# Kernel optimization log

Hardware: AMD Instinct MI355X
Metric: run time of the kernel (lower is better)

## Reference

```python
import jax, jax.numpy as jnp
import numpy as np

B, L, DM, H, DK, DV = 4, 1024, 1024, 16, 64, 64


def setup_inputs() -> dict:
    key = jax.random.key(0)
    ks = jax.random.split(key, 9)
    s = 0.02
    q = jax.random.normal(ks[0], (B, L, DM), jnp.float32)
    k = jax.random.normal(ks[1], (B, L, DM), jnp.float32)
    v = jax.random.normal(ks[2], (B, L, DM), jnp.float32)
    # causal mask: True = masked out
    attn_mask = jnp.broadcast_to(jnp.triu(jnp.ones((L, L), bool), k=1), (B, L, L))
    w_q = jax.random.normal(ks[3], (DM, H * DK), jnp.float32) * s
    w_k = jax.random.normal(ks[4], (DM, H * DK), jnp.float32) * s
    w_v = jax.random.normal(ks[5], (DM, H * DV), jnp.float32) * s
    w_o = jax.random.normal(ks[6], (H * DV, DM), jnp.float32) * s
    ln_g = jnp.ones((DM,), jnp.float32)
    ln_b = jnp.zeros((DM,), jnp.float32)
    return {"q": q, "k": k, "v": v, "w_q": w_q, "w_k": w_k, "w_v": w_v,
            "w_o": w_o, "ln_g": ln_g, "ln_b": ln_b,
            "attn_mask": attn_mask, "n_head": H}


def _mha(q, k, v, w_q, w_k, w_v, w_o, ln_g, ln_b, attn_mask, n_head):
    b, lq, dm = q.shape
    lk = k.shape[1]
    d_k = w_q.shape[1] // n_head
    d_v = w_v.shape[1] // n_head
    temper = jnp.asarray(np.sqrt(dm), q.dtype)  # NOTE: sqrt(d_model), as in source
    residual = q
    # faithful to source: flat .view reshape (b, l, h*d) -> (b*h, l, d), NO transpose
    qh = (q @ w_q).reshape(b * n_head, lq, d_k)
    kh = (k @ w_k).reshape(b * n_head, lk, d_k)
    vh = (v @ w_v).reshape(b * n_head, lk, d_v)
    attn = jnp.einsum('bqd,bkd->bqk', qh, kh) / temper  # (b*h, lq, lk)
    mask_r = jnp.tile(attn_mask, (n_head, 1, 1))
    attn = jnp.where(mask_r, -jnp.inf, attn)
    attn = jax.nn.softmax(attn, axis=-1)
    out = jnp.einsum('bqk,bkd->bqd', attn, vh)  # (b*h, lq, d_v)
    out = out.reshape(b, lq, n_head * d_v)
    out = out @ w_o + residual  # dropout = identity (eval)
    mu = jnp.mean(out, axis=-1, keepdims=True)
    var = jnp.mean(jnp.square(out - mu), axis=-1, keepdims=True)
    out = (out - mu) * jax.lax.rsqrt(var + 1e-6) * ln_g + ln_b
    return out, attn


def reference(q, k, v, w_q, w_k, w_v, w_o, ln_g, ln_b, attn_mask, n_head):
    return _mha(q, k, v, w_q, w_k, w_v, w_o, ln_g, ln_b, attn_mask, n_head)
```

## Files before the change

### kernel.cpp

```cpp
#include <hip/hip_runtime.h>
#include <stdint.h>

typedef unsigned short u16;
typedef __attribute__((ext_vector_type(8))) short bf16x8;
typedef __attribute__((ext_vector_type(4))) float f32x4;
typedef __attribute__((ext_vector_type(4))) unsigned short us4;

#define MFMA_BF16(a, b, c) __builtin_amdgcn_mfma_f32_16x16x32_bf16((a), (b), (c), 0, 0, 0)

__device__ __forceinline__ u16 f2bf(float f) {
  uint32_t u = __builtin_bit_cast(uint32_t, f);
  u += 0x7fffu + ((u >> 16) & 1u);
  return (u16)(u >> 16);
}

__device__ __forceinline__ void async_copy16(void* lds, const void* g) {
  __builtin_amdgcn_global_load_lds(
      (const __attribute__((address_space(1))) unsigned int*)g,
      (__attribute__((address_space(3))) unsigned int*)lds, 16, 0, 0);
}

__global__ __launch_bounds__(256) void k_pre(const float* __restrict__ q,
                                             const float* __restrict__ k,
                                             const float* __restrict__ v,
                                             const float* __restrict__ w0,
                                             const float* __restrict__ w1,
                                             const float* __restrict__ w2,
                                             const float* __restrict__ w3,
                                             us4* __restrict__ qkvb,
                                             u16* __restrict__ wT) {
  __shared__ float t[32][33];
  int bid = blockIdx.x;
  int tid = threadIdx.x;
  if (bid < 12288) {
    int z = bid >> 12;
    const float4* src = (z == 0) ? (const float4*)q : (z == 1) ? (const float4*)k : (const float4*)v;
    int i = (bid & 4095) * 256 + tid;
    float4 val = src[i];
    us4 o;
    o[0] = f2bf(val.x); o[1] = f2bf(val.y); o[2] = f2bf(val.z); o[3] = f2bf(val.w);
    qkvb[(size_t)z * 1048576 + i] = o;
  } else {
    int w = bid - 12288;
    int z = w >> 10, r_ = w & 1023;
    int bx = r_ & 31, by = r_ >> 5;
    const float* W = (z == 0) ? w0 : (z == 1) ? w1 : (z == 2) ? w2 : w3;
    u16* WT = wT + (size_t)z * 1048576;
    int c = tid & 31, r0 = tid >> 5;
#pragma unroll
    for (int i = 0; i < 4; ++i) {
      int r = r0 + i * 8;
      t[r][c] = W[(size_t)(by * 32 + r) * 1024 + bx * 32 + c];
    }
    __syncthreads();
#pragma unroll
    for (int i = 0; i < 4; ++i) {
      int r = r0 + i * 8;
      WT[(size_t)(bx * 32 + r) * 1024 + by * 32 + c] = f2bf(t[c][r]);
    }
  }
}

__global__ __launch_bounds__(256) void k_vtrans(const u16* __restrict__ VP, u16* __restrict__ VT) {
  int jt = blockIdx.x;
  int bh = blockIdx.y;
  __shared__ u16 t[64][65];
  int tid = threadIdx.x;
  const u16* src = VP + (size_t)bh * 65536 + (size_t)jt * 64 * 64;
#pragma unroll
  for (int i = 0; i < 16; ++i) {
    int e = tid + i * 256;
    t[e >> 6][e & 63] = src[e];
  }
  __syncthreads();
  u16* dst = VT + (size_t)bh * 65536 + jt * 64;
#pragma unroll
  for (int i = 0; i < 16; ++i) {
    int e = tid + i * 256;
    int d = e >> 6, j = e & 63;
    dst[(size_t)d * 1024 + j] = t[j][d];
  }
}

__global__ __launch_bounds__(256) void k_gemm_bt(const u16* __restrict__ A,
                                                 const u16* __restrict__ BT,
                                                 u16* __restrict__ Cb, float* __restrict__ Cf,
                                                 const float* __restrict__ res,
                                                 int N, int K, int mode, int wgrp) {
  __shared__ __align__(16) u16 SM[4][4096];
  int bm, bn;
  {
    int wg = blockIdx.x + blockIdx.y * gridDim.x;
    int per = gridDim.y >> 3;
    int xcd = wg & 7;
    int idx = wg >> 3;
    bm = xcd * per + (idx % per);
    bn = idx / per;
  }
  int tid = threadIdx.x;
  int wave = tid >> 6, lane = tid & 63;
  int wr = wave >> 1, wc = wave & 1;
  int fl = lane & 15, fg = lane >> 4;
  f32x4 acc[4][4] = {};

  const char* Abase = (const char*)(A + (size_t)bm * 128 * K);
  const char* Bbase = (const char*)(BT + (wgrp ? (size_t)(bm >> 5) * 1048576 : 0) +
                                    (size_t)bn * 128 * K);
  int off = wave * 1024 + lane * 16;

#define GSTAGE(buf, kt)                                                              \
  {                                                                                  \
    _Pragma("unroll") for (int is = 0; is < 2; ++is) {                               \
      int o = is * 4096 + off;                                                       \
      int row = o >> 6, cb = o & 63;                                                 \
      async_copy16((char*)SM[buf] + is * 4096 + wave * 1024,                         \
                   Abase + (size_t)row * (K * 2) + (kt) * 2 + cb);                   \
      async_copy16((char*)SM[2 + (buf)] + is * 4096 + wave * 1024,                   \
                   Bbase + (size_t)row * (K * 2) + (kt) * 2 + cb);                   \
    }                                                                                \
  }

  GSTAGE(0, 0);
  __syncthreads();
  int cur = 0;
  for (int kt = 0; kt < K; kt += 32) {
    if (kt + 32 < K) GSTAGE(cur ^ 1, kt + 32);
    bf16x8 af[4], bfr[4];
#pragma unroll
    for (int m = 0; m < 4; ++m)
      af[m] = *(const bf16x8*)((const char*)SM[cur] + (wr * 64 + m * 16 + fl) * 64 + fg * 16);
#pragma unroll
    for (int n = 0; n < 4; ++n)
      bfr[n] = *(const bf16x8*)((const char*)SM[2 + cur] + (wc * 64 + n * 16 + fl) * 64 + fg * 16);
#pragma unroll
    for (int m = 0; m < 4; ++m)
#pragma unroll
      for (int n = 0; n < 4; ++n)
        acc[m][n] = MFMA_BF16(af[m], bfr[n], acc[m][n]);
    __syncthreads();
    cur ^= 1;
  }
#undef GSTAGE

  float* EP = (float*)&SM[0][0] + wave * 2048;
  int colbase = bn * 128 + wc * 64;
#pragma unroll
  for (int m = 0; m < 4; ++m) {
    int rowbase = bm * 128 + wr * 64 + m * 16;
#pragma unroll
    for (int n = 0; n < 4; ++n)
#pragma unroll
      for (int r = 0; r < 4; ++r)
        EP[(fg * 4 + r) * 68 + n * 16 + fl] = acc[m][n][r];
    if (mode) {
#pragma unroll
      for (int j = 0; j < 4; ++j) {
        int row = (lane >> 4) + 4 * j;
        int colf = (lane & 15) * 4;
        float4 val = *(const float4*)(&EP[row * 68 + colf]);
        size_t gidx = (size_t)(rowbase + row) * N + colbase + colf;
        float4 rr = *(const float4*)(res + gidx);
        val.x += rr.x; val.y += rr.y; val.z += rr.z; val.w += rr.w;
        *(float4*)(Cf + gidx) = val;
      }
    } else {
#pragma unroll
      for (int j = 0; j < 2; ++j) {
        int row = (lane >> 3) + 8 * j;
        int colf = (lane & 7) * 8;
        const float* s = &EP[row * 68 + colf];
        us4 lo, hi;
#pragma unroll
        for (int i = 0; i < 4; ++i) { lo[i] = f2bf(s[i]); hi[i] = f2bf(s[4 + i]); }
        u16* d = Cb + (size_t)(rowbase + row) * N + colbase + colf;
        *(us4*)d = lo;
        *(us4*)(d + 4) = hi;
      }
    }
  }
}

__global__ __launch_bounds__(256) void k_gemm_out64(const u16* __restrict__ A,
                                                    const u16* __restrict__ BT,
                                                    float* __restrict__ Cf,
                                                    const float* __restrict__ res) {
  __shared__ __align__(16) u16 SM[12288];
  char* base = (char*)SM;
  int bm, bn;
  {
    int wg = blockIdx.x + blockIdx.y * 8;
    int xcd = wg & 7, idx = wg >> 3;
    bm = xcd * 8 + (idx & 7);
    bn = idx >> 3;
  }
  int tid = threadIdx.x;
  int wave = tid >> 6, lane = tid & 63;
  int wr = wave >> 1, wc = wave & 1;
  int fl = lane & 15, fg = lane >> 4;
  f32x4 acc[2][4] = {};

  const char* Abase = (const char*)(A + (size_t)bm * 65536);
  const char* Bbase = (const char*)(BT + (size_t)bn * 131072);

#define OSTAGE(buf, kt)                                                          \
  {                                                                              \
    int oA = wave * 1024 + lane * 16;                                            \
    int rowA = oA >> 6, cbA = oA & 63;                                           \
    async_copy16(base + (buf) * 4096 + wave * 1024,                              \
                 Abase + (size_t)rowA * 2048 + (kt) * 2 + cbA);                  \
    _Pragma("unroll") for (int is = 0; is < 2; ++is) {                           \
      int oB = is * 4096 + wave * 1024 + lane * 16;                              \
      int rowB = oB >> 6, cbB = oB & 63;                                         \
      async_copy16(base + 8192 + (buf) * 8192 + is * 4096 + wave * 1024,         \
                   Bbase + (size_t)rowB * 2048 + (kt) * 2 + cbB);                \
    }                                                                            \
  }

  OSTAGE(0, 0);
  __syncthreads();
  int cur = 0;
  for (int kt = 0; kt < 1024; kt += 32) {
    if (kt + 32 < 1024) OSTAGE(cur ^ 1, kt + 32);
    const char* Ab = base + cur * 4096;
    const char* Bb = base + 8192 + cur * 8192;
    bf16x8 af[2], bfr[4];
#pragma unroll
    for (int m = 0; m < 2; ++m)
      af[m] = *(const bf16x8*)(Ab + (wr * 32 + m * 16 + fl) * 64 + fg * 16);
#pragma unroll
    for (int n = 0; n < 4; ++n)
      bfr[n] = *(const bf16x8*)(Bb + (wc * 64 + n * 16 + fl) * 64 + fg * 16);
#pragma unroll
    for (int m = 0; m < 2; ++m)
#pragma unroll
      for (int n = 0; n < 4; ++n)
        acc[m][n] = MFMA_BF16(af[m], bfr[n], acc[m][n]);
    __syncthreads();
    cur ^= 1;
  }
#undef OSTAGE

  float* EP = (float*)base + wave * 1088;
  int colbase = bn * 128 + wc * 64;
#pragma unroll
  for (int m = 0; m < 2; ++m) {
    int rowbase = bm * 64 + wr * 32 + m * 16;
#pragma unroll
    for (int n = 0; n < 4; ++n)
#pragma unroll
      for (int r = 0; r < 4; ++r)
        EP[(fg * 4 + r) * 68 + n * 16 + fl] = acc[m][n][r];
#pragma unroll
    for (int j = 0; j < 4; ++j) {
      int row = (lane >> 4) + 4 * j;
      int colf = (lane & 15) * 4;
      float4 val = *(const float4*)(&EP[row * 68 + colf]);
      size_t gidx = (size_t)(rowbase + row) * 1024 + colbase + colf;
      float4 rr = *(const float4*)(res + gidx);
      val.x += rr.x; val.y += rr.y; val.z += rr.z; val.w += rr.w;
      *(float4*)(Cf + gidx) = val;
    }
  }
}

__global__ __launch_bounds__(256) void k_attn(const u16* __restrict__ QP,
                                              const u16* __restrict__ KP,
                                              const u16* __restrict__ VT,
                                              float* __restrict__ attn,
                                              u16* __restrict__ AO) {
  int bh = blockIdx.x;
  int qb = 15 - blockIdx.y;
  int tid = threadIdx.x;
  int wave = tid >> 6, lane = tid & 63;
  int fl = lane & 15, fg = lane >> 4;
  int qw = qb * 64 + wave * 16;

  const u16* Qb = QP + (size_t)bh * 65536;
  const char* Kbyte = (const char*)(KP + (size_t)bh * 65536);
  const u16* Vb = VT + (size_t)bh * 65536;
  float* Ab = attn + (size_t)bh * 1048576;

  __shared__ __align__(16) u16 Ks[2][4096];
  __shared__ __align__(16) float Ps[4][16][36];
  __shared__ __align__(16) u16 Pt[4][16][64];

#define KSTAGE(buf, jt)                                                                 \
  {                                                                                     \
    _Pragma("unroll") for (int c2 = 0; c2 < 2; ++c2) {                                  \
      int o = c2 * 4096 + wave * 1024 + lane * 16;                                      \
      int row = o >> 7, col = o & 127;                                                  \
      async_copy16((char*)Ks[buf] + c2 * 4096 + wave * 1024,                            \
                   Kbyte + (size_t)((jt) * 64 + row) * 128 + (col ^ ((row & 7) << 4))); \
    }                                                                                   \
  }

  bf16x8 qf0 = *(const bf16x8*)(Qb + (size_t)(qw + fl) * 64 + fg * 8);
  bf16x8 qf1 = *(const bf16x8*)(Qb + (size_t)(qw + fl) * 64 + 32 + fg * 8);

  float den[4] = {0.f, 0.f, 0.f, 0.f};

  KSTAGE(0, 0);
  __syncthreads();
  int cur = 0;
  for (int jt = 0; jt <= qb; ++jt) {
    if (jt < qb) KSTAGE(cur ^ 1, jt + 1);
    int j0 = jt * 64;
    f32x4 c[4] = {};
#pragma unroll
    for (int n = 0; n < 4; ++n) {
      int r = n * 16 + fl;
      bf16x8 k0 = *(const bf16x8*)((const char*)Ks[cur] + r * 128 + ((fg * 16) ^ ((r & 7) << 4)));
      bf16x8 k1 = *(const bf16x8*)((const char*)Ks[cur] + r * 128 + ((64 + fg * 16) ^ ((r & 7) << 4)));
      c[n] = MFMA_BF16(qf0, k0, c[n]);
      c[n] = MFMA_BF16(qf1, k1, c[n]);
    }
#pragma unroll
    for (int r = 0; r < 4; ++r) {
      int row = qw + fg * 4 + r;
      float sum = 0.f;
#pragma unroll
      for (int n = 0; n < 4; ++n) {
        int col = j0 + n * 16 + fl;
        sum += (col > row) ? 0.f : __expf(c[n][r] * 0.03125f);
      }
#pragma unroll
      for (int o2 = 1; o2 < 16; o2 <<= 1) sum += __shfl_xor(sum, o2);
      den[r] += sum;
    }
    __syncthreads();
    cur ^= 1;
  }

  float invden[4];
#pragma unroll
  for (int r = 0; r < 4; ++r) invden[r] = 1.0f / den[r];

  f32x4 oacc[4] = {};

  KSTAGE(0, 0);
  __syncthreads();
  cur = 0;
  for (int jt = 0; jt <= qb; ++jt) {
    if (jt < qb) KSTAGE(cur ^ 1, jt + 1);
    int j0 = jt * 64;
    f32x4 c[4] = {};
#pragma unroll
    for (int n = 0; n < 4; ++n) {
      int r = n * 16 + fl;
      bf16x8 k0 = *(const bf16x8*)((const char*)Ks[cur] + r * 128 + ((fg * 16) ^ ((r & 7) << 4)));
      bf16x8 k1 = *(const bf16x8*)((const char*)Ks[cur] + r * 128 + ((64 + fg * 16) ^ ((r & 7) << 4)));
      c[n] = MFMA_BF16(qf0, k0, c[n]);
      c[n] = MFMA_BF16(qf1, k1, c[n]);
    }
    bf16x8 vf0[4], vf1[4];
#pragma unroll
    for (int n = 0; n < 4; ++n) {
      const u16* vp = Vb + (size_t)(n * 16 + fl) * 1024 + j0;
      vf0[n] = *(const bf16x8*)(vp + fg * 8);
      vf1[n] = *(const bf16x8*)(vp + 32 + fg * 8);
    }
    float pv_[4][4];
#pragma unroll
    for (int r = 0; r < 4; ++r) {
      int row = qw + fg * 4 + r;
#pragma unroll
      for (int n = 0; n < 4; ++n) {
        int col = j0 + n * 16 + fl;
        pv_[n][r] = (col > row) ? 0.f : __expf(c[n][r] * 0.03125f) * invden[r];
      }
    }
#pragma unroll
    for (int t = 0; t < 2; ++t) {
#pragma unroll
      for (int n2 = 0; n2 < 2; ++n2)
#pragma unroll
        for (int r = 0; r < 4; ++r)
          Ps[wave][fg * 4 + r][n2 * 16 + fl] = pv_[t * 2 + n2][r];
#pragma unroll
      for (int i = 0; i < 2; ++i) {
        int idx = i * 64 + lane;
        int r16 = idx >> 3, f4 = idx & 7;
        float4 val = *(const float4*)(&Ps[wave][r16][f4 * 4]);
        *(float4*)(Ab + (size_t)(qw + r16) * 1024 + j0 + t * 32 + f4 * 4) = val;
      }
    }
#pragma unroll
    for (int r = 0; r < 4; ++r)
#pragma unroll
      for (int n = 0; n < 4; ++n)
        Pt[wave][fg * 4 + r][n * 16 + fl] = f2bf(pv_[n][r]);
    bf16x8 pa0 = *(const bf16x8*)(&Pt[wave][fl][fg * 8]);
    bf16x8 pa1 = *(const bf16x8*)(&Pt[wave][fl][32 + fg * 8]);
#pragma unroll
    for (int n = 0; n < 4; ++n) {
      oacc[n] = MFMA_BF16(pa0, vf0[n], oacc[n]);
      oacc[n] = MFMA_BF16(pa1, vf1[n], oacc[n]);
    }
    __syncthreads();
    cur ^= 1;
  }
#undef KSTAGE

  float4 z; z.x = 0.f; z.y = 0.f; z.z = 0.f; z.w = 0.f;
  for (int jt = qb + 1; jt < 16; ++jt) {
    int j0 = jt * 64;
#pragma unroll
    for (int i = 0; i < 4; ++i) {
      int idx = i * 64 + lane;
      int r16 = idx >> 4, f4 = idx & 15;
      *(float4*)(Ab + (size_t)(qw + r16) * 1024 + j0 + f4 * 4) = z;
    }
  }

#pragma unroll
  for (int n = 0; n < 4; ++n)
#pragma unroll
    for (int r = 0; r < 4; ++r)
      Pt[wave][fg * 4 + r][n * 16 + fl] = f2bf(oacc[n][r]);
#pragma unroll
  for (int j = 0; j < 2; ++j) {
    int row = (lane >> 3) + 8 * j;
    int colf = (lane & 7) * 8;
    bf16x8 val = *(const bf16x8*)(&Pt[wave][row][colf]);
    *(bf16x8*)(AO + (size_t)bh * 65536 + (size_t)(qw + row) * 64 + colf) = val;
  }
}

__global__ __launch_bounds__(256) void k_lnorm(float* __restrict__ io,
                                               const float* __restrict__ g,
                                               const float* __restrict__ b) {
  int row = blockIdx.x, tid = threadIdx.x;
  float* p = io + (size_t)row * 1024 + tid * 4;
  float4 x = *(const float4*)p;
  float s1 = x.x + x.y + x.z + x.w;
  float s2 = x.x * x.x + x.y * x.y + x.z * x.z + x.w * x.w;
#pragma unroll
  for (int o = 1; o < 64; o <<= 1) {
    s1 += __shfl_xor(s1, o);
    s2 += __shfl_xor(s2, o);
  }
  __shared__ float r1[4], r2[4];
  int wave = tid >> 6;
  if ((tid & 63) == 0) { r1[wave] = s1; r2[wave] = s2; }
  __syncthreads();
  s1 = r1[0] + r1[1] + r1[2] + r1[3];
  s2 = r2[0] + r2[1] + r2[2] + r2[3];
  float mu = s1 * (1.0f / 1024.0f);
  float var = s2 * (1.0f / 1024.0f) - mu * mu;
  float rs = rsqrtf(var + 1e-6f);
  float4 gg = *(const float4*)(g + tid * 4);
  float4 bb = *(const float4*)(b + tid * 4);
  float4 y;
  y.x = (x.x - mu) * rs * gg.x + bb.x;
  y.y = (x.y - mu) * rs * gg.y + bb.y;
  y.z = (x.z - mu) * rs * gg.z + bb.z;
  y.w = (x.w - mu) * rs * gg.w + bb.w;
  *(float4*)p = y;
}

extern "C" void kernel_launch(void* const* d_in, const int* in_sizes, int n_in,
                              void* d_out, int out_size, void* d_ws, size_t ws_size,
                              hipStream_t stream) {
  const float* q = (const float*)d_in[0];
  const float* k = (const float*)d_in[1];
  const float* v = (const float*)d_in[2];
  const float* w_q = (const float*)d_in[3];
  const float* w_k = (const float*)d_in[4];
  const float* w_v = (const float*)d_in[5];
  const float* w_o = (const float*)d_in[6];
  const float* ln_g = (const float*)d_in[7];
  const float* ln_b = (const float*)d_in[8];

  float* out = (float*)d_out;
  float* attnp = out + 4194304;

  char* ws = (char*)d_ws;
  u16* QP = (u16*)(ws);
  u16* VP = (u16*)(ws + (16u << 20));
  u16* VT = (u16*)(ws + (24u << 20));
  u16* AO = (u16*)(ws + (32u << 20));
  u16* wT = (u16*)(ws + (40u << 20));
  u16* KP = QP + 4194304;
  u16* woT = wT + 3145728;

  u16* qkvb = (u16*)attnp;

  k_pre<<<16384, 256, 0, stream>>>(q, k, v, w_q, w_k, w_v, w_o, (us4*)qkvb, wT);

  k_gemm_bt<<<dim3(8, 96), 256, 0, stream>>>(qkvb, wT, QP, nullptr, nullptr, 1024, 1024, 0, 1);

  k_vtrans<<<dim3(16, 64), 256, 0, stream>>>(VP, VT);

  k_attn<<<dim3(64, 16), 256, 0, stream>>>(QP, KP, VT, attnp, AO);

  k_gemm_out64<<<dim3(8, 64), 256, 0, stream>>>(AO, woT, out, q);

  k_lnorm<<<4096, 256, 0, stream>>>(out, ln_g, ln_b);
}
```

Before: 160.3 us.

## Load K directly from global memory and drop LDS double-buffering in attention

Removes the LDS K staging (async global-to-LDS copies, double buffer, and per-tile __syncthreads) from both attention passes. Each wave now reads its K fragments straight from global memory, relying on L1/L2 reuse across the four waves. The V fragment loads move next to the PV MFMAs, and __expf(x/32) becomes exp2f(x*log2e/32). This removes barriers and LDS traffic but repeats global K reads per wave and exposes load latency with no explicit prefetch.

```diff
diff --git a/kernel.cpp b/kernel.cpp
--- a/kernel.cpp
+++ b/kernel.cpp
@@ -276,41 +276,28 @@
   int qw = qb * 64 + wave * 16;
 
   const u16* Qb = QP + (size_t)bh * 65536;
-  const char* Kbyte = (const char*)(KP + (size_t)bh * 65536);
+  const u16* Kb = KP + (size_t)bh * 65536;
   const u16* Vb = VT + (size_t)bh * 65536;
   float* Ab = attn + (size_t)bh * 1048576;
 
-  __shared__ __align__(16) u16 Ks[2][4096];
   __shared__ __align__(16) float Ps[4][16][36];
   __shared__ __align__(16) u16 Pt[4][16][64];
 
-#define KSTAGE(buf, jt)                                                                 \
-  {                                                                                     \
-    _Pragma("unroll") for (int c2 = 0; c2 < 2; ++c2) {                                  \
-      int o = c2 * 4096 + wave * 1024 + lane * 16;                                      \
-      int row = o >> 7, col = o & 127;                                                  \
-      async_copy16((char*)Ks[buf] + c2 * 4096 + wave * 1024,                            \
-                   Kbyte + (size_t)((jt) * 64 + row) * 128 + (col ^ ((row & 7) << 4))); \
-    }                                                                                   \
-  }
+  const float K2 = 0.045084220f;
 
   bf16x8 qf0 = *(const bf16x8*)(Qb + (size_t)(qw + fl) * 64 + fg * 8);
   bf16x8 qf1 = *(const bf16x8*)(Qb + (size_t)(qw + fl) * 64 + 32 + fg * 8);
 
   float den[4] = {0.f, 0.f, 0.f, 0.f};
 
-  KSTAGE(0, 0);
-  __syncthreads();
-  int cur = 0;
   for (int jt = 0; jt <= qb; ++jt) {
-    if (jt < qb) KSTAGE(cur ^ 1, jt + 1);
     int j0 = jt * 64;
     f32x4 c[4] = {};
 #pragma unroll
     for (int n = 0; n < 4; ++n) {
-      int r = n * 16 + fl;
-      bf16x8 k0 = *(const bf16x8*)((const char*)Ks[cur] + r * 128 + ((fg * 16) ^ ((r & 7) << 4)));
-      bf16x8 k1 = *(const bf16x8*)((const char*)Ks[cur] + r * 128 + ((64 + fg * 16) ^ ((r & 7) << 4)));
+      const u16* kp = Kb + (size_t)(j0 + n * 16 + fl) * 64;
+      bf16x8 k0 = *(const bf16x8*)(kp + fg * 8);
+      bf16x8 k1 = *(const bf16x8*)(kp + 32 + fg * 8);
       c[n] = MFMA_BF16(qf0, k0, c[n]);
       c[n] = MFMA_BF16(qf1, k1, c[n]);
     }
@@ -321,14 +308,12 @@
 #pragma unroll
       for (int n = 0; n < 4; ++n) {
         int col = j0 + n * 16 + fl;
-        sum += (col > row) ? 0.f : __expf(c[n][r] * 0.03125f);
+        sum += (col > row) ? 0.f : exp2f(c[n][r] * K2);
       }
 #pragma unroll
       for (int o2 = 1; o2 < 16; o2 <<= 1) sum += __shfl_xor(sum, o2);
       den[r] += sum;
     }
-    __syncthreads();
-    cur ^= 1;
   }
 
   float invden[4];
@@ -337,28 +322,17 @@
 
   f32x4 oacc[4] = {};
 
-  KSTAGE(0, 0);
-  __syncthreads();
-  cur = 0;
   for (int jt = 0; jt <= qb; ++jt) {
-    if (jt < qb) KSTAGE(cur ^ 1, jt + 1);
     int j0 = jt * 64;
     f32x4 c[4] = {};
 #pragma unroll
     for (int n = 0; n < 4; ++n) {
-      int r = n * 16 + fl;
-      bf16x8 k0 = *(const bf16x8*)((const char*)Ks[cur] + r * 128 + ((fg * 16) ^ ((r & 7) << 4)));
-      bf16x8 k1 = *(const bf16x8*)((const char*)Ks[cur] + r * 128 + ((64 + fg * 16) ^ ((r & 7) << 4)));
+      const u16* kp = Kb + (size_t)(j0 + n * 16 + fl) * 64;
+      bf16x8 k0 = *(const bf16x8*)(kp + fg * 8);
+      bf16x8 k1 = *(const bf16x8*)(kp + 32 + fg * 8);
       c[n] = MFMA_BF16(qf0, k0, c[n]);
       c[n] = MFMA_BF16(qf1, k1, c[n]);
     }
-    bf16x8 vf0[4], vf1[4];
-#pragma unroll
-    for (int n = 0; n < 4; ++n) {
-      const u16* vp = Vb + (size_t)(n * 16 + fl) * 1024 + j0;
-      vf0[n] = *(const bf16x8*)(vp + fg * 8);
-      vf1[n] = *(const bf16x8*)(vp + 32 + fg * 8);
-    }
     float pv_[4][4];
 #pragma unroll
     for (int r = 0; r < 4; ++r) {
@@ -366,7 +340,7 @@
 #pragma unroll
       for (int n = 0; n < 4; ++n) {
         int col = j0 + n * 16 + fl;
-        pv_[n][r] = (col > row) ? 0.f : __expf(c[n][r] * 0.03125f) * invden[r];
+        pv_[n][r] = (col > row) ? 0.f : exp2f(c[n][r] * K2) * invden[r];
       }
     }
 #pragma unroll
@@ -393,13 +367,13 @@
     bf16x8 pa1 = *(const bf16x8*)(&Pt[wave][fl][32 + fg * 8]);
 #pragma unroll
     for (int n = 0; n < 4; ++n) {
-      oacc[n] = MFMA_BF16(pa0, vf0[n], oacc[n]);
-      oacc[n] = MFMA_BF16(pa1, vf1[n], oacc[n]);
-    }
-    __syncthreads();
-    cur ^= 1;
-  }
-#undef KSTAGE
+      const u16* vp = Vb + (size_t)(n * 16 + fl) * 1024 + j0;
+      bf16x8 v0 = *(const bf16x8*)(vp + fg * 8);
+      bf16x8 v1 = *(const bf16x8*)(vp + 32 + fg * 8);
+      oacc[n] = MFMA_BF16(pa0, v0, oacc[n]);
+      oacc[n] = MFMA_BF16(pa1, v1, oacc[n]);
+    }
+  }
 
   float4 z; z.x = 0.f; z.y = 0.f; z.z = 0.f; z.w = 0.f;
   for (int jt = qb + 1; jt < 16; ++jt) {
```

Result: slower. 215.2 us (+34.2%).

## Overlap causal-mask zero-fill of attention output with the QKV projection GEMM

Applied to the files above, without the earlier changes.

The QKV GEMM grid gains extra blocks, interleaved among the GEMM tiles. These blocks zero the strictly-upper-triangular tiles of the attention-probability output for heads 6 and up, whose memory is not used as bf16 staging for the projection inputs. The attention kernel now zero-fills only heads 0–5, so most of the large store traffic overlaps with the compute-bound GEMM instead of running in the attention kernel. The GEMM is also specialised to fixed sizes, and the softmax uses exp2f with a folded log2(e)/32 constant instead of __expf. In exchange, the buffer aliasing becomes more fragile and the tile-to-XCD mapping gets more complex.

```diff
diff --git a/kernel.cpp b/kernel.cpp
--- a/kernel.cpp
+++ b/kernel.cpp
@@ -82,30 +82,47 @@
   }
 }
 
-__global__ __launch_bounds__(256) void k_gemm_bt(const u16* __restrict__ A,
-                                                 const u16* __restrict__ BT,
-                                                 u16* __restrict__ Cb, float* __restrict__ Cf,
-                                                 const float* __restrict__ res,
-                                                 int N, int K, int mode, int wgrp) {
+__global__ __launch_bounds__(256) void k_gemm_qkv(const u16* __restrict__ A,
+                                                  const u16* __restrict__ BT,
+                                                  u16* __restrict__ Cb,
+                                                  float* __restrict__ attnp) {
   __shared__ __align__(16) u16 SM[4][4096];
-  int bm, bn;
-  {
-    int wg = blockIdx.x + blockIdx.y * gridDim.x;
-    int per = gridDim.y >> 3;
-    int xcd = wg & 7;
-    int idx = wg >> 3;
-    bm = xcd * per + (idx % per);
-    bn = idx / per;
-  }
   int tid = threadIdx.x;
+  int wg = blockIdx.x + blockIdx.y * 8;
+  int xcd = wg & 7;
+  int idx = wg >> 3;
+  int gi_cur = (idx * 96) / 154;
+  int gi_next = ((idx + 1) * 96) / 154;
+  if (gi_next == gi_cur) {
+    int zi = idx - gi_cur;
+    int unit = xcd * 58 + zi;
+    int bh = 6 + (unit >> 3);
+    int s = unit & 7;
+    float* Ah = attnp + (size_t)bh * 1048576;
+    float4 z4; z4.x = 0.f; z4.y = 0.f; z4.z = 0.f; z4.w = 0.f;
+    for (int qb2 = 0; qb2 < 15; ++qb2)
+      for (int jt = qb2 + 1; jt < 16; ++jt) {
+        if (((qb2 * 16 + jt) & 7) != s) continue;
+        float* basez = Ah + (size_t)(qb2 * 64) * 1024 + jt * 64;
+#pragma unroll
+        for (int i = 0; i < 4; ++i) {
+          int id2 = i * 256 + tid;
+          int row = id2 >> 4, c16 = id2 & 15;
+          *(float4*)(basez + (size_t)row * 1024 + c16 * 4) = z4;
+        }
+      }
+    return;
+  }
+  int gi = gi_cur;
+  int bm = xcd * 12 + (gi % 12);
+  int bn = gi / 12;
   int wave = tid >> 6, lane = tid & 63;
   int wr = wave >> 1, wc = wave & 1;
   int fl = lane & 15, fg = lane >> 4;
   f32x4 acc[4][4] = {};
 
-  const char* Abase = (const char*)(A + (size_t)bm * 128 * K);
-  const char* Bbase = (const char*)(BT + (wgrp ? (size_t)(bm >> 5) * 1048576 : 0) +
-                                    (size_t)bn * 128 * K);
+  const char* Abase = (const char*)(A + (size_t)bm * 131072);
+  const char* Bbase = (const char*)(BT + (size_t)(bm >> 5) * 1048576 + (size_t)bn * 131072);
   int off = wave * 1024 + lane * 16;
 
 #define GSTAGE(buf, kt)                                                              \
@@ -114,17 +131,17 @@
       int o = is * 4096 + off;                                                       \
       int row = o >> 6, cb = o & 63;                                                 \
       async_copy16((char*)SM[buf] + is * 4096 + wave * 1024,                         \
-                   Abase + (size_t)row * (K * 2) + (kt) * 2 + cb);                   \
+                   Abase + (size_t)row * 2048 + (kt) * 2 + cb);                      \
       async_copy16((char*)SM[2 + (buf)] + is * 4096 + wave * 1024,                   \
-                   Bbase + (size_t)row * (K * 2) + (kt) * 2 + cb);                   \
+                   Bbase + (size_t)row * 2048 + (kt) * 2 + cb);                      \
     }                                                                                \
   }
 
   GSTAGE(0, 0);
   __syncthreads();
   int cur = 0;
-  for (int kt = 0; kt < K; kt += 32) {
-    if (kt + 32 < K) GSTAGE(cur ^ 1, kt + 32);
+  for (int kt = 0; kt < 1024; kt += 32) {
+    if (kt + 32 < 1024) GSTAGE(cur ^ 1, kt + 32);
     bf16x8 af[4], bfr[4];
 #pragma unroll
     for (int m = 0; m < 4; ++m)
@@ -152,30 +169,17 @@
 #pragma unroll
       for (int r = 0; r < 4; ++r)
         EP[(fg * 4 + r) * 68 + n * 16 + fl] = acc[m][n][r];
-    if (mode) {
-#pragma unroll
-      for (int j = 0; j < 4; ++j) {
-        int row = (lane >> 4) + 4 * j;
-        int colf = (lane & 15) * 4;
-        float4 val = *(const float4*)(&EP[row * 68 + colf]);
-        size_t gidx = (size_t)(rowbase + row) * N + colbase + colf;
-        float4 rr = *(const float4*)(res + gidx);
-        val.x += rr.x; val.y += rr.y; val.z += rr.z; val.w += rr.w;
-        *(float4*)(Cf + gidx) = val;
-      }
-    } else {
-#pragma unroll
-      for (int j = 0; j < 2; ++j) {
-        int row = (lane >> 3) + 8 * j;
-        int colf = (lane & 7) * 8;
-        const float* s = &EP[row * 68 + colf];
-        us4 lo, hi;
-#pragma unroll
-        for (int i = 0; i < 4; ++i) { lo[i] = f2bf(s[i]); hi[i] = f2bf(s[4 + i]); }
-        u16* d = Cb + (size_t)(rowbase + row) * N + colbase + colf;
-        *(us4*)d = lo;
-        *(us4*)(d + 4) = hi;
-      }
+#pragma unroll
+    for (int j = 0; j < 2; ++j) {
+      int row = (lane >> 3) + 8 * j;
+      int colf = (lane & 7) * 8;
+      const float* s = &EP[row * 68 + colf];
+      us4 lo, hi;
+#pragma unroll
+      for (int i = 0; i < 4; ++i) { lo[i] = f2bf(s[i]); hi[i] = f2bf(s[4 + i]); }
+      u16* d = Cb + (size_t)(rowbase + row) * 1024 + colbase + colf;
+      *(us4*)d = lo;
+      *(us4*)(d + 4) = hi;
     }
   }
 }
@@ -284,6 +288,8 @@
   __shared__ __align__(16) float Ps[4][16][36];
   __shared__ __align__(16) u16 Pt[4][16][64];
 
+  const float K2 = 0.045084220f;
+
 #define KSTAGE(buf, jt)                                                                 \
   {                                                                                     \
     _Pragma("unroll") for (int c2 = 0; c2 < 2; ++c2) {                                  \
@@ -321,7 +327,7 @@
 #pragma unroll
       for (int n = 0; n < 4; ++n) {
         int col = j0 + n * 16 + fl;
-        sum += (col > row) ? 0.f : __expf(c[n][r] * 0.03125f);
+        sum += (col > row) ? 0.f : exp2f(c[n][r] * K2);
       }
 #pragma unroll
       for (int o2 = 1; o2 < 16; o2 <<= 1) sum += __shfl_xor(sum, o2);
@@ -366,7 +372,7 @@
 #pragma unroll
       for (int n = 0; n < 4; ++n) {
         int col = j0 + n * 16 + fl;
-        pv_[n][r] = (col > row) ? 0.f : __expf(c[n][r] * 0.03125f) * invden[r];
+        pv_[n][r] = (col > row) ? 0.f : exp2f(c[n][r] * K2) * invden[r];
       }
     }
 #pragma unroll
@@ -401,14 +407,16 @@
   }
 #undef KSTAGE
 
-  float4 z; z.x = 0.f; z.y = 0.f; z.z = 0.f; z.w = 0.f;
-  for (int jt = qb + 1; jt < 16; ++jt) {
-    int j0 = jt * 64;
-#pragma unroll
-    for (int i = 0; i < 4; ++i) {
-      int idx = i * 64 + lane;
-      int r16 = idx >> 4, f4 = idx & 15;
-      *(float4*)(Ab + (size_t)(qw + r16) * 1024 + j0 + f4 * 4) = z;
+  if (bh < 6) {
+    float4 z; z.x = 0.f; z.y = 0.f; z.z = 0.f; z.w = 0.f;
+    for (int jt = qb + 1; jt < 16; ++jt) {
+      int j0 = jt * 64;
+#pragma unroll
+      for (int i = 0; i < 4; ++i) {
+        int idx = i * 64 + lane;
+        int r16 = idx >> 4, f4 = idx & 15;
+        *(float4*)(Ab + (size_t)(qw + r16) * 1024 + j0 + f4 * 4) = z;
+      }
     }
   }
 
@@ -487,7 +495,7 @@
 
   k_pre<<<16384, 256, 0, stream>>>(q, k, v, w_q, w_k, w_v, w_o, (us4*)qkvb, wT);
 
-  k_gemm_bt<<<dim3(8, 96), 256, 0, stream>>>(qkvb, wT, QP, nullptr, nullptr, 1024, 1024, 0, 1);
+  k_gemm_qkv<<<dim3(8, 154), 256, 0, stream>>>(qkvb, wT, QP, attnp);
 
   k_vtrans<<<dim3(16, 64), 256, 0, stream>>>(VP, VT);
 
```

After: 180.1 us. 12.4% more time.

## Fuse fp32-to-bf16 activation conversion into QKV GEMM and use exp2 softmax

Applied to the files above, without the earlier changes.

The separate pre-pass that converted q/k/v to bf16 is removed. The QKV GEMM now loads fp32 activation tiles directly into swizzled LDS and converts them to bf16 in registers with packed cvt instructions, so the intermediate bf16 activation buffer is never written or read back. The weight transpose becomes its own kernel. Separately, the softmax exponent uses exp2f with a folded log2e scale. In exchange, A-tile LDS traffic doubles and conversion ALU work moves into the GEMM inner loop.

```diff
diff --git a/kernel.cpp b/kernel.cpp
--- a/kernel.cpp
+++ b/kernel.cpp
@@ -20,44 +20,37 @@
       (__attribute__((address_space(3))) unsigned int*)lds, 16, 0, 0);
 }
 
-__global__ __launch_bounds__(256) void k_pre(const float* __restrict__ q,
-                                             const float* __restrict__ k,
-                                             const float* __restrict__ v,
-                                             const float* __restrict__ w0,
-                                             const float* __restrict__ w1,
-                                             const float* __restrict__ w2,
-                                             const float* __restrict__ w3,
-                                             us4* __restrict__ qkvb,
-                                             u16* __restrict__ wT) {
+__device__ __forceinline__ bf16x8 cvt8(f32x4 lo, f32x4 hi) {
+  union { bf16x8 v; uint32_t w[4]; } u;
+  asm("v_cvt_pk_bf16_f32 %0, %1, %2" : "=v"(u.w[0]) : "v"(lo[0]), "v"(lo[1]));
+  asm("v_cvt_pk_bf16_f32 %0, %1, %2" : "=v"(u.w[1]) : "v"(lo[2]), "v"(lo[3]));
+  asm("v_cvt_pk_bf16_f32 %0, %1, %2" : "=v"(u.w[2]) : "v"(hi[0]), "v"(hi[1]));
+  asm("v_cvt_pk_bf16_f32 %0, %1, %2" : "=v"(u.w[3]) : "v"(hi[2]), "v"(hi[3]));
+  return u.v;
+}
+
+__global__ __launch_bounds__(256) void k_pre_w(const float* __restrict__ w0,
+                                               const float* __restrict__ w1,
+                                               const float* __restrict__ w2,
+                                               const float* __restrict__ w3,
+                                               u16* __restrict__ wT) {
+  const float* W = (blockIdx.z == 0) ? w0 : (blockIdx.z == 1) ? w1
+                   : (blockIdx.z == 2) ? w2 : w3;
+  u16* WT = wT + (size_t)blockIdx.z * 1048576;
   __shared__ float t[32][33];
-  int bid = blockIdx.x;
+  int bx = blockIdx.x, by = blockIdx.y;
   int tid = threadIdx.x;
-  if (bid < 12288) {
-    int z = bid >> 12;
-    const float4* src = (z == 0) ? (const float4*)q : (z == 1) ? (const float4*)k : (const float4*)v;
-    int i = (bid & 4095) * 256 + tid;
-    float4 val = src[i];
-    us4 o;
-    o[0] = f2bf(val.x); o[1] = f2bf(val.y); o[2] = f2bf(val.z); o[3] = f2bf(val.w);
-    qkvb[(size_t)z * 1048576 + i] = o;
-  } else {
-    int w = bid - 12288;
-    int z = w >> 10, r_ = w & 1023;
-    int bx = r_ & 31, by = r_ >> 5;
-    const float* W = (z == 0) ? w0 : (z == 1) ? w1 : (z == 2) ? w2 : w3;
-    u16* WT = wT + (size_t)z * 1048576;
-    int c = tid & 31, r0 = tid >> 5;
-#pragma unroll
-    for (int i = 0; i < 4; ++i) {
-      int r = r0 + i * 8;
-      t[r][c] = W[(size_t)(by * 32 + r) * 1024 + bx * 32 + c];
-    }
-    __syncthreads();
-#pragma unroll
-    for (int i = 0; i < 4; ++i) {
-      int r = r0 + i * 8;
-      WT[(size_t)(bx * 32 + r) * 1024 + by * 32 + c] = f2bf(t[c][r]);
-    }
+  int c = tid & 31, r0 = tid >> 5;
+#pragma unroll
+  for (int i = 0; i < 4; ++i) {
+    int r = r0 + i * 8;
+    t[r][c] = W[(size_t)(by * 32 + r) * 1024 + bx * 32 + c];
+  }
+  __syncthreads();
+#pragma unroll
+  for (int i = 0; i < 4; ++i) {
+    int r = r0 + i * 8;
+    WT[(size_t)(bx * 32 + r) * 1024 + by * 32 + c] = f2bf(t[c][r]);
   }
 }
 
@@ -82,16 +75,17 @@
   }
 }
 
-__global__ __launch_bounds__(256) void k_gemm_bt(const u16* __restrict__ A,
-                                                 const u16* __restrict__ BT,
-                                                 u16* __restrict__ Cb, float* __restrict__ Cf,
-                                                 const float* __restrict__ res,
-                                                 int N, int K, int mode, int wgrp) {
-  __shared__ __align__(16) u16 SM[4][4096];
+__global__ __launch_bounds__(256) void k_gemm_qkv(const float* __restrict__ q,
+                                                  const float* __restrict__ k,
+                                                  const float* __restrict__ v,
+                                                  const u16* __restrict__ wT,
+                                                  u16* __restrict__ Cb) {
+  __shared__ __align__(16) float Asm[2][4096];
+  __shared__ __align__(16) u16 Bsm[2][4096];
   int bm, bn;
   {
-    int wg = blockIdx.x + blockIdx.y * gridDim.x;
-    int per = gridDim.y >> 3;
+    int wg = blockIdx.x + blockIdx.y * 8;
+    int per = 12;
     int xcd = wg & 7;
     int idx = wg >> 3;
     bm = xcd * per + (idx % per);
@@ -103,35 +97,51 @@
   int fl = lane & 15, fg = lane >> 4;
   f32x4 acc[4][4] = {};
 
-  const char* Abase = (const char*)(A + (size_t)bm * 128 * K);
-  const char* Bbase = (const char*)(BT + (wgrp ? (size_t)(bm >> 5) * 1048576 : 0) +
-                                    (size_t)bn * 128 * K);
-  int off = wave * 1024 + lane * 16;
-
-#define GSTAGE(buf, kt)                                                              \
-  {                                                                                  \
-    _Pragma("unroll") for (int is = 0; is < 2; ++is) {                               \
-      int o = is * 4096 + off;                                                       \
-      int row = o >> 6, cb = o & 63;                                                 \
-      async_copy16((char*)SM[buf] + is * 4096 + wave * 1024,                         \
-                   Abase + (size_t)row * (K * 2) + (kt) * 2 + cb);                   \
-      async_copy16((char*)SM[2 + (buf)] + is * 4096 + wave * 1024,                   \
-                   Bbase + (size_t)row * (K * 2) + (kt) * 2 + cb);                   \
-    }                                                                                \
-  }
-
-  GSTAGE(0, 0);
+  int z = bm >> 5;
+  const char* Abase = (const char*)((z == 0 ? q : z == 1 ? k : v) + (size_t)(bm & 31) * 131072);
+  const char* Bbase = (const char*)(wT + (size_t)z * 1048576 + (size_t)bn * 131072);
+
+#define ASTAGE(buf, kt)                                                             \
+  {                                                                                 \
+    _Pragma("unroll") for (int is = 0; is < 4; ++is) {                              \
+      int o = is * 4096 + wave * 1024 + lane * 16;                                  \
+      int row = o >> 7, cb = o & 127;                                               \
+      async_copy16((char*)Asm[buf] + is * 4096 + wave * 1024,                       \
+                   Abase + (size_t)row * 4096 + (kt) * 4 + (cb ^ ((row & 7) << 4))); \
+    }                                                                               \
+  }
+#define BSTAGE(buf, kt)                                                             \
+  {                                                                                 \
+    _Pragma("unroll") for (int is = 0; is < 2; ++is) {                              \
+      int o = is * 4096 + wave * 1024 + lane * 16;                                  \
+      int row = o >> 6, cb = o & 63;                                                \
+      async_copy16((char*)Bsm[buf] + is * 4096 + wave * 1024,                       \
+                   Bbase + (size_t)row * 2048 + (kt) * 2 + cb);                     \
+    }                                                                               \
+  }
+
+  ASTAGE(0, 0);
+  BSTAGE(0, 0);
   __syncthreads();
   int cur = 0;
-  for (int kt = 0; kt < K; kt += 32) {
-    if (kt + 32 < K) GSTAGE(cur ^ 1, kt + 32);
+  for (int kt = 0; kt < 1024; kt += 32) {
+    if (kt + 32 < 1024) {
+      ASTAGE(cur ^ 1, kt + 32);
+      BSTAGE(cur ^ 1, kt + 32);
+    }
     bf16x8 af[4], bfr[4];
 #pragma unroll
-    for (int m = 0; m < 4; ++m)
-      af[m] = *(const bf16x8*)((const char*)SM[cur] + (wr * 64 + m * 16 + fl) * 64 + fg * 16);
+    for (int m = 0; m < 4; ++m) {
+      int R = wr * 64 + m * 16 + fl;
+      const char* ar = (const char*)Asm[cur] + R * 128;
+      int s = (R & 7) << 4;
+      f32x4 lo = *(const f32x4*)(ar + ((fg * 32) ^ s));
+      f32x4 hi = *(const f32x4*)(ar + ((fg * 32 + 16) ^ s));
+      af[m] = cvt8(lo, hi);
+    }
 #pragma unroll
     for (int n = 0; n < 4; ++n)
-      bfr[n] = *(const bf16x8*)((const char*)SM[2 + cur] + (wc * 64 + n * 16 + fl) * 64 + fg * 16);
+      bfr[n] = *(const bf16x8*)((const char*)Bsm[cur] + (wc * 64 + n * 16 + fl) * 64 + fg * 16);
 #pragma unroll
     for (int m = 0; m < 4; ++m)
 #pragma unroll
@@ -140,9 +150,10 @@
     __syncthreads();
     cur ^= 1;
   }
-#undef GSTAGE
-
-  float* EP = (float*)&SM[0][0] + wave * 2048;
+#undef ASTAGE
+#undef BSTAGE
+
+  float* EP = (float*)&Asm[0][0] + wave * 1088;
   int colbase = bn * 128 + wc * 64;
 #pragma unroll
   for (int m = 0; m < 4; ++m) {
@@ -152,30 +163,17 @@
 #pragma unroll
       for (int r = 0; r < 4; ++r)
         EP[(fg * 4 + r) * 68 + n * 16 + fl] = acc[m][n][r];
-    if (mode) {
-#pragma unroll
-      for (int j = 0; j < 4; ++j) {
-        int row = (lane >> 4) + 4 * j;
-        int colf = (lane & 15) * 4;
-        float4 val = *(const float4*)(&EP[row * 68 + colf]);
-        size_t gidx = (size_t)(rowbase + row) * N + colbase + colf;
-        float4 rr = *(const float4*)(res + gidx);
-        val.x += rr.x; val.y += rr.y; val.z += rr.z; val.w += rr.w;
-        *(float4*)(Cf + gidx) = val;
-      }
-    } else {
-#pragma unroll
-      for (int j = 0; j < 2; ++j) {
-        int row = (lane >> 3) + 8 * j;
-        int colf = (lane & 7) * 8;
-        const float* s = &EP[row * 68 + colf];
-        us4 lo, hi;
-#pragma unroll
-        for (int i = 0; i < 4; ++i) { lo[i] = f2bf(s[i]); hi[i] = f2bf(s[4 + i]); }
-        u16* d = Cb + (size_t)(rowbase + row) * N + colbase + colf;
-        *(us4*)d = lo;
-        *(us4*)(d + 4) = hi;
-      }
+#pragma unroll
+    for (int j = 0; j < 2; ++j) {
+      int row = (lane >> 3) + 8 * j;
+      int colf = (lane & 7) * 8;
+      const float* s = &EP[row * 68 + colf];
+      us4 lo, hi;
+#pragma unroll
+      for (int i = 0; i < 4; ++i) { lo[i] = f2bf(s[i]); hi[i] = f2bf(s[4 + i]); }
+      u16* d = Cb + (size_t)(rowbase + row) * 1024 + colbase + colf;
+      *(us4*)d = lo;
+      *(us4*)(d + 4) = hi;
     }
   }
 }
@@ -284,6 +282,8 @@
   __shared__ __align__(16) float Ps[4][16][36];
   __shared__ __align__(16) u16 Pt[4][16][64];
 
+  const float K2 = 0.045084220f;
+
 #define KSTAGE(buf, jt)                                                                 \
   {                                                                                     \
     _Pragma("unroll") for (int c2 = 0; c2 < 2; ++c2) {                                  \
@@ -321,7 +321,7 @@
 #pragma unroll
       for (int n = 0; n < 4; ++n) {
         int col = j0 + n * 16 + fl;
-        sum += (col > row) ? 0.f : __expf(c[n][r] * 0.03125f);
+        sum += (col > row) ? 0.f : exp2f(c[n][r] * K2);
       }
 #pragma unroll
       for (int o2 = 1; o2 < 16; o2 <<= 1) sum += __shfl_xor(sum, o2);
@@ -366,7 +366,7 @@
 #pragma unroll
       for (int n = 0; n < 4; ++n) {
         int col = j0 + n * 16 + fl;
-        pv_[n][r] = (col > row) ? 0.f : __expf(c[n][r] * 0.03125f) * invden[r];
+        pv_[n][r] = (col > row) ? 0.f : exp2f(c[n][r] * K2) * invden[r];
       }
     }
 #pragma unroll
@@ -483,11 +483,9 @@
   u16* KP = QP + 4194304;
   u16* woT = wT + 3145728;
 
-  u16* qkvb = (u16*)attnp;
-
-  k_pre<<<16384, 256, 0, stream>>>(q, k, v, w_q, w_k, w_v, w_o, (us4*)qkvb, wT);
-
-  k_gemm_bt<<<dim3(8, 96), 256, 0, stream>>>(qkvb, wT, QP, nullptr, nullptr, 1024, 1024, 0, 1);
+  k_pre_w<<<dim3(32, 32, 4), 256, 0, stream>>>(w_q, w_k, w_v, w_o, wT);
+
+  k_gemm_qkv<<<dim3(8, 96), 256, 0, stream>>>(q, k, v, wT, QP);
 
   k_vtrans<<<dim3(16, 64), 256, 0, stream>>>(VP, VT);
 
```

After: 167.8 us. 1.05x slower.
